# Kernel optimization log

Measured on AMD Instinct MI355X. Metric: run time of the kernel, lower is better.

The kernel has to match this reference:

```python
import jax, jax.numpy as jnp
import numpy as np


def setup_inputs() -> dict:
    key = jax.random.key(0)
    ks = jax.random.split(key, 7)
    B, D, d1, d2, d3 = 256, 256, 1024, 512, 256
    s = lambda f: 1.0 / np.sqrt(f)  # torch nn.Linear-style init scale
    return {
        "x": jax.random.normal(ks[0], (B, D), jnp.float32),
        "W1": jax.random.normal(ks[1], (d1, D), jnp.float32) * s(D),
        "b1": jax.random.normal(ks[2], (d1,), jnp.float32) * s(D),
        "W2": jax.random.normal(ks[3], (d2, d1), jnp.float32) * s(d1),
        "b2": jax.random.normal(ks[4], (d2,), jnp.float32) * s(d1),
        "W3": jax.random.normal(ks[5], (d3, d2), jnp.float32) * s(d2),
        "b3": jax.random.normal(ks[6], (d3,), jnp.float32) * s(d2),
        "k": 10,
    }


def _border_dists(x, W1, b1, W2, b2, W3, b3):
    # Layer 1: pre-activations and boundary distances. For the first layer the
    # effective linear map is W1 itself (shared across the batch).
    z1 = x @ W1.T + b1                                   # [B, d1]
    dist1 = jnp.abs(z1) / jnp.linalg.norm(W1, axis=1)    # [B, d1]
    m1 = (z1 > 0).astype(x.dtype)
    V1 = m1[:, :, None] * W1[None]                       # [B, d1, D] per-instance map after ReLU
    h1 = m1 * z1

    # Layer 2
    z2 = h1 @ W2.T + b2                                  # [B, d2]
    V2 = jnp.einsum('oi,bid->bod', W2, V1)               # [B, d2, D]
    dist2 = jnp.abs(z2) / jnp.linalg.norm(V2, axis=2)
    m2 = (z2 > 0).astype(x.dtype)
    h2 = m2 * z2

    # Layer 3
    z3 = h2 @ W3.T + b3                                  # [B, d3]
    V3 = jnp.einsum('oi,bid->bod', W3, m2[:, :, None] * V2)  # [B, d3, D]
    dist3 = jnp.abs(z3) / jnp.linalg.norm(V3, axis=2)

    return jnp.concatenate([dist1, dist2, dist3], axis=1)  # [B, d1+d2+d3]


def reference(x, W1, b1, W2, b2, W3, b3, k):
    dists = _border_dists(x, W1, b1, W2, b2, W3, b3)
    # smallest-k distances per instance via top_k on negated distances
    neg_top, _ = jax.lax.top_k(-dists, k)                # [B, k]
    return jnp.sum(-neg_top)                             # border-distance loss (scalar)
```

## Files before the change

### kernel.cpp

```cpp
#include <hip/hip_runtime.h>
#include <math.h>
#include <float.h>

#define B   256
#define D   256
#define D1  1024
#define D2  512
#define D3  256
#define NDIST (D1 + D2 + D3)
#define CQ  2.0f

typedef __attribute__((ext_vector_type(8))) short short8;
typedef __attribute__((ext_vector_type(4))) float f32x4;
typedef __attribute__((ext_vector_type(4))) int   i32x4;

__device__ __forceinline__ float waveReduceSum(float v) {
    #pragma unroll
    for (int off = 32; off > 0; off >>= 1)
        v += __shfl_down(v, off, 64);
    return v;
}
__device__ __forceinline__ float waveReduceMax(float v) {
    #pragma unroll
    for (int off = 32; off > 0; off >>= 1)
        v = fmaxf(v, __shfl_down(v, off, 64));
    return v;
}

__device__ __forceinline__ unsigned short f2bf(float f) {
    unsigned int u = __float_as_uint(f);
    u = (u + 0x7FFFu + ((u >> 16) & 1u)) >> 16;
    return (unsigned short)u;
}
__device__ __forceinline__ float bf2f(unsigned short h) {
    return __uint_as_float(((unsigned int)h) << 16);
}
__device__ __forceinline__ void gld16(const void* g, void* l) {
    __builtin_amdgcn_global_load_lds(
        (const __attribute__((address_space(1))) unsigned int*)g,
        (__attribute__((address_space(3))) unsigned int*)l, 16, 0, 0);
}

__device__ __forceinline__ int swz_src(int row, int lane) {
    return ((lane & 3) + ((row >> 1) & 3)) & 3;
}
__device__ __forceinline__ int swz_frag(int row, int quad) {
    return row * 32 + (((quad - ((row >> 1) & 3)) & 3) * 8);
}

__global__ __launch_bounds__(256) void k_prep(
    const float* __restrict__ x,  const float* __restrict__ W1,
    const float* __restrict__ W2, const float* __restrict__ W3,
    float* __restrict__ zeros,
    float* __restrict__ outp,
    unsigned short* __restrict__ xhi,  unsigned short* __restrict__ xlo,
    unsigned short* __restrict__ W1hi, unsigned short* __restrict__ W1lo,
    unsigned short* __restrict__ W2hi, unsigned short* __restrict__ W2lo,
    unsigned short* __restrict__ W3hi, unsigned short* __restrict__ W3lo,
    signed char* __restrict__ W1Ti8, float* __restrict__ saq,
    signed char* __restrict__ W2i8,  float* __restrict__ sbq,
    signed char* __restrict__ W3i8,  float* __restrict__ s3q,
    float* __restrict__ rn1) {
    int blk = blockIdx.x;
    int t = threadIdx.x;
    if (blk < 1536) {
        if (blk == 0 && t == 0) outp[0] = 0.f;
        zeros[blk * 256 + t] = 0.f;
        return;
    }
    if (blk < 2496) {
        int i4 = ((blk - 1536) * 256 + t) * 4;
        const float* src; unsigned short *hi, *lo; int off;
        if (i4 < 65536)       { src = x;  hi = xhi;  lo = xlo;  off = i4; }
        else if (i4 < 327680) { src = W1; hi = W1hi; lo = W1lo; off = i4 - 65536; }
        else if (i4 < 851968) { src = W2; hi = W2hi; lo = W2lo; off = i4 - 327680; }
        else                  { src = W3; hi = W3hi; lo = W3lo; off = i4 - 851968; }
        float4 v = *(const float4*)(src + off);
        ushort4 h, l;
        h.x = f2bf(v.x); l.x = f2bf(v.x - bf2f(h.x));
        h.y = f2bf(v.y); l.y = f2bf(v.y - bf2f(h.y));
        h.z = f2bf(v.z); l.z = f2bf(v.z - bf2f(h.z));
        h.w = f2bf(v.w); l.w = f2bf(v.w - bf2f(h.w));
        *(ushort4*)(hi + off) = h;
        *(ushort4*)(lo + off) = l;
        return;
    }
    if (blk < 2528) {
        int ty = t >> 5, tx = t & 31;
        int d = (blk - 2496) * 8 + ty;
        float m = 0.f;
        for (int i = tx; i < D1; i += 32) m = fmaxf(m, fabsf(W1[(size_t)i * D + d]));
        #pragma unroll
        for (int off = 16; off > 0; off >>= 1) m = fmaxf(m, __shfl_down(m, off, 32));
        m = __shfl(m, 0, 32);
        m = fmaxf(m, 1e-20f);
        if (tx == 0) saq[d] = m / 127.f;
        float inv = 127.f / m;
        for (int i = tx; i < D1; i += 32) {
            int q = __float2int_rn(W1[(size_t)i * D + d] * inv);
            W1Ti8[(size_t)d * D1 + i] = (signed char)q;
        }
        return;
    }
    if (blk < 2656) {
        int o = (blk - 2528) * 4 + (t >> 6);
        int l = t & 63;
        const float* row = W2 + (size_t)o * D1;
        float m = 0.f;
        for (int tt = l; tt < D1; tt += 64) m = fmaxf(m, fabsf(row[tt]));
        m = waveReduceMax(m);
        m = __shfl(m, 0, 64);
        m = fmaxf(m, 1e-20f);
        if (l == 0) sbq[o] = m / 127.f;
        float inv = 127.f / m;
        for (int tt = l; tt < D1; tt += 64)
            W2i8[(size_t)o * D1 + tt] = (signed char)__float2int_rn(row[tt] * inv);
        return;
    }
    if (blk < 2720) {
        int p = (blk - 2656) * 4 + (t >> 6);
        int l = t & 63;
        const float* row = W3 + (size_t)p * D2;
        float m = 0.f;
        for (int tt = l; tt < D2; tt += 64) m = fmaxf(m, fabsf(row[tt]));
        m = waveReduceMax(m);
        m = __shfl(m, 0, 64);
        m = fmaxf(m, 1e-20f);
        if (l == 0) s3q[p] = m / 127.f;
        float inv = 127.f / m;
        for (int tt = l; tt < D2; tt += 64)
            W3i8[(size_t)p * D2 + tt] = (signed char)__float2int_rn(row[tt] * inv);
        return;
    }
    {
        int gw = (blk - 2720) * 4 + (t >> 6);
        int lane = t & 63;
        const float* row = W1 + (size_t)gw * D;
        float s = 0.f;
        for (int tt = lane; tt < D; tt += 64) { float v = row[tt]; s += v * v; }
        s = waveReduceSum(s);
        if (lane == 0) rn1[gw] = sqrtf(s);
    }
}

template <int KD, int KL>
__device__ __forceinline__ void mfma3_64(
    const unsigned short* __restrict__ Ahi, const unsigned short* __restrict__ Alo,
    const unsigned short* __restrict__ Bhi, const unsigned short* __restrict__ Blo,
    int m0, int n0, int k0, unsigned short* sm, f32x4 acc[2][2]) {
    int tid = threadIdx.x;
    int l = tid & 63, w = tid >> 6;
    int rsub = l >> 2;
    int quad = l >> 4, l16 = l & 15;
    int wm = (w >> 1) * 32, wn = (w & 1) * 32;
    unsigned short* sAh = sm;
    unsigned short* sAl = sm + 2048;
    unsigned short* sBh = sm + 4096;
    unsigned short* sBl = sm + 6144;
    ptrdiff_t dA = Alo - Ahi, dB = Blo - Bhi;
    int rloc = w * 16 + rsub;
    int c = swz_src(rloc, l);
    const unsigned short* pa = Ahi + (size_t)(m0 + rloc) * KD + k0 + c * 8;
    const unsigned short* pb = Bhi + (size_t)(n0 + rloc) * KD + k0 + c * 8;
    int aoff[2], boff[2];
    #pragma unroll
    for (int mt = 0; mt < 2; mt++) aoff[mt] = swz_frag(wm + mt * 16 + l16, quad);
    #pragma unroll
    for (int nt = 0; nt < 2; nt++) boff[nt] = swz_frag(wn + nt * 16 + l16, quad);
    for (int kk = 0; kk < KL; kk += 32) {
        gld16(pa + kk,      sAh + w * 512);
        gld16(pa + dA + kk, sAl + w * 512);
        gld16(pb + kk,      sBh + w * 512);
        gld16(pb + dB + kk, sBl + w * 512);
        __syncthreads();
        short8 ah[2], al[2], bh[2], bl[2];
        #pragma unroll
        for (int mt = 0; mt < 2; mt++) {
            ah[mt] = *(const short8*)(sAh + aoff[mt]);
            al[mt] = *(const short8*)(sAl + aoff[mt]);
        }
        #pragma unroll
        for (int nt = 0; nt < 2; nt++) {
            bh[nt] = *(const short8*)(sBh + boff[nt]);
            bl[nt] = *(const short8*)(sBl + boff[nt]);
        }
        #pragma unroll
        for (int mt = 0; mt < 2; mt++)
            #pragma unroll
            for (int nt = 0; nt < 2; nt++) {
                acc[mt][nt] = __builtin_amdgcn_mfma_f32_16x16x32_bf16(ah[mt], bh[nt], acc[mt][nt], 0, 0, 0);
                acc[mt][nt] = __builtin_amdgcn_mfma_f32_16x16x32_bf16(ah[mt], bl[nt], acc[mt][nt], 0, 0, 0);
                acc[mt][nt] = __builtin_amdgcn_mfma_f32_16x16x32_bf16(al[mt], bh[nt], acc[mt][nt], 0, 0, 0);
            }
        __syncthreads();
    }
}

__global__ __launch_bounds__(256) void k_l1(
    const unsigned short* __restrict__ xhi,  const unsigned short* __restrict__ xlo,
    const unsigned short* __restrict__ W1hi, const unsigned short* __restrict__ W1lo,
    const float* __restrict__ b1, const float* __restrict__ rn1,
    float* __restrict__ dists, unsigned char* __restrict__ m1q,
    unsigned short* __restrict__ h1hi, unsigned short* __restrict__ h1lo) {
    __shared__ __align__(16) unsigned short sm[8192];
    int m0 = blockIdx.x * 64, n0 = blockIdx.y * 64;
    f32x4 acc[2][2] = {};
    mfma3_64<D, D>(xhi, xlo, W1hi, W1lo, m0, n0, 0, sm, acc);
    int l = threadIdx.x & 63, w = threadIdx.x >> 6;
    int quad = l >> 4, l16 = l & 15;
    int wm = (w >> 1) * 32, wn = (w & 1) * 32;
    #pragma unroll
    for (int mt = 0; mt < 2; mt++)
        #pragma unroll
        for (int nt = 0; nt < 2; nt++) {
            int n = n0 + wn + nt * 16 + l16;
            float bv = b1[n], rv = rn1[n];
            #pragma unroll
            for (int r = 0; r < 4; r++) {
                int m = m0 + wm + mt * 16 + quad * 4 + r;
                float z = acc[mt][nt][r] + bv;
                size_t idx = (size_t)m * D1 + n;
                dists[idx] = fabsf(z) / rv;
                m1q[idx] = (z > 0.f) ? 0xFFu : 0u;
                float h = z > 0.f ? z : 0.f;
                unsigned short hh = f2bf(h);
                h1hi[idx] = hh;
                h1lo[idx] = f2bf(h - bf2f(hh));
            }
        }
}

__global__ __launch_bounds__(256) void k_l2a(
    const unsigned short* __restrict__ h1hi, const unsigned short* __restrict__ h1lo,
    const unsigned short* __restrict__ W2hi, const unsigned short* __restrict__ W2lo,
    float* __restrict__ z2) {
    __shared__ __align__(16) unsigned short sm[8192];
    int m0 = blockIdx.x * 64, n0 = blockIdx.y * 64, k0 = blockIdx.z * 256;
    f32x4 acc[2][2] = {};
    mfma3_64<D1, 256>(h1hi, h1lo, W2hi, W2lo, m0, n0, k0, sm, acc);
    int l = threadIdx.x & 63, w = threadIdx.x >> 6;
    int quad = l >> 4, l16 = l & 15;
    int wm = (w >> 1) * 32, wn = (w & 1) * 32;
    #pragma unroll
    for (int mt = 0; mt < 2; mt++)
        #pragma unroll
        for (int nt = 0; nt < 2; nt++) {
            int n = n0 + wn + nt * 16 + l16;
            #pragma unroll
            for (int r = 0; r < 4; r++) {
                int m = m0 + wm + mt * 16 + quad * 4 + r;
                atomicAdd(&z2[(size_t)m * D2 + n], acc[mt][nt][r]);
            }
        }
}

__global__ __launch_bounds__(256) void k_l2b(
    const float* __restrict__ b2, float* __restrict__ z2,
    unsigned char* __restrict__ m2q,
    unsigned short* __restrict__ h2hi, unsigned short* __restrict__ h2lo) {
    int idx = blockIdx.x * 256 + threadIdx.x;
    int n = idx & (D2 - 1);
    float z = z2[idx] + b2[n];
    z2[idx] = z;
    m2q[idx] = (z > 0.f) ? 0xFFu : 0u;
    float h = z > 0.f ? z : 0.f;
    unsigned short hh = f2bf(h);
    h2hi[idx] = hh;
    h2lo[idx] = f2bf(h - bf2f(hh));
}

__global__ __launch_bounds__(256) void k_l3a(
    const unsigned short* __restrict__ h2hi, const unsigned short* __restrict__ h2lo,
    const unsigned short* __restrict__ W3hi, const unsigned short* __restrict__ W3lo,
    float* __restrict__ z3) {
    __shared__ __align__(16) unsigned short sm[8192];
    int m0 = blockIdx.x * 64, n0 = blockIdx.y * 64, k0 = blockIdx.z * 256;
    f32x4 acc[2][2] = {};
    mfma3_64<D2, 256>(h2hi, h2lo, W3hi, W3lo, m0, n0, k0, sm, acc);
    int l = threadIdx.x & 63, w = threadIdx.x >> 6;
    int quad = l >> 4, l16 = l & 15;
    int wm = (w >> 1) * 32, wn = (w & 1) * 32;
    #pragma unroll
    for (int mt = 0; mt < 2; mt++)
        #pragma unroll
        for (int nt = 0; nt < 2; nt++) {
            int n = n0 + wn + nt * 16 + l16;
            #pragma unroll
            for (int r = 0; r < 4; r++) {
                int m = m0 + wm + mt * 16 + quad * 4 + r;
                atomicAdd(&z3[(size_t)m * D3 + n], acc[mt][nt][r]);
            }
        }
}

__global__ __launch_bounds__(256) void k_l3b(
    const float* __restrict__ b3, float* __restrict__ z3) {
    int idx = blockIdx.x * 256 + threadIdx.x;
    z3[idx] = z3[idx] + b3[idx & (D3 - 1)];
}

__global__ __launch_bounds__(256) void k_gemm1(
    const signed char* __restrict__ W1Ti8,
    const signed char* __restrict__ W2i8,
    const unsigned char* __restrict__ m1q,
    const float* __restrict__ saq,
    const float* __restrict__ sbq,
    signed char* __restrict__ qV2,
    float* __restrict__ norm2,
    int b0) {
    __shared__ __align__(16) signed char As[16384];
    __shared__ __align__(16) signed char Bs[16384];
    int m0 = blockIdx.x * 128;
    int o0 = blockIdx.y * 128;
    int bc = blockIdx.z;
    int b = b0 + bc;
    int tid = threadIdx.x;
    int l = tid & 63, w = tid >> 6;
    int quad = l >> 4, l16 = l & 15;
    int wm = (w >> 1) * 64, wn = (w & 1) * 64;
    const unsigned char* mrow = m1q + (size_t)b * D1;

    const signed char* pa[4];
    const signed char* pb[4];
    int lrow = l >> 3, ls = l & 7;
    #pragma unroll
    for (int r = 0; r < 4; r++) {
        int row = r * 32 + w * 8 + lrow;
        int c = (ls + (row & 7)) & 7;
        pa[r] = W1Ti8 + (size_t)(m0 + row) * D1 + c * 16;
        pb[r] = W2i8 + (size_t)(o0 + row) * D1 + c * 16;
    }
    int aoff[4][2], boff[4][2];
    #pragma unroll
    for (int mt = 0; mt < 4; mt++) {
        int tr = wm + mt * 16 + l16;
        #pragma unroll
        for (int ks = 0; ks < 2; ks++)
            aoff[mt][ks] = tr * 128 + (((ks * 4 + quad) - (tr & 7)) & 7) * 16;
    }
    #pragma unroll
    for (int nt = 0; nt < 4; nt++) {
        int tr = wn + nt * 16 + l16;
        #pragma unroll
        for (int ks = 0; ks < 2; ks++)
            boff[nt][ks] = tr * 128 + (((ks * 4 + quad) - (tr & 7)) & 7) * 16;
    }

    i32x4 acc[4][4];
    #pragma unroll
    for (int i = 0; i < 4; i++)
        #pragma unroll
        for (int j = 0; j < 4; j++) acc[i][j] = (i32x4)0;

    for (int kk = 0; kk < D1; kk += 128) {
        #pragma unroll
        for (int r = 0; r < 4; r++) {
            gld16(pa[r] + kk, As + r * 4096 + w * 1024);
            gld16(pb[r] + kk, Bs + r * 4096 + w * 1024);
        }
        i32x4 mv0 = *(const i32x4*)(mrow + kk + quad * 16);
        i32x4 mv1 = *(const i32x4*)(mrow + kk + 64 + quad * 16);
        __syncthreads();
        #pragma unroll
        for (int ks = 0; ks < 2; ks++) {
            i32x4 mv = ks ? mv1 : mv0;
            i32x4 a[4], bq[4];
            #pragma unroll
            for (int mt = 0; mt < 4; mt++)
                a[mt] = (*(const i32x4*)(As + aoff[mt][ks])) & mv;
            #pragma unroll
            for (int nt = 0; nt < 4; nt++)
                bq[nt] = *(const i32x4*)(Bs + boff[nt][ks]);
            #pragma unroll
            for (int mt = 0; mt < 4; mt++)
                #pragma unroll
                for (int nt = 0; nt < 4; nt++)
                    acc[mt][nt] = __builtin_amdgcn_mfma_i32_16x16x64_i8(
                        a[mt], bq[nt], acc[mt][nt], 0, 0, 0);
        }
        __syncthreads();
    }

    float sad[4][4];
    #pragma unroll
    for (int mt = 0; mt < 4; mt++)
        #pragma unroll
        for (int r = 0; r < 4; r++)
            sad[mt][r] = saq[m0 + wm + mt * 16 + quad * 4 + r];
    float sbv[4], sbdq[4];
    #pragma unroll
    for (int nt = 0; nt < 4; nt++) {
        sbv[nt] = sbq[o0 + wn + nt * 16 + l16];
        sbdq[nt] = sbv[nt] * (1.0f / CQ);
    }

    #pragma unroll
    for (int nt = 0; nt < 4; nt++) {
        float s = 0.f;
        #pragma unroll
        for (int mt = 0; mt < 4; mt++)
            #pragma unroll
            for (int r = 0; r < 4; r++) {
                float v = (float)acc[mt][nt][r] * sad[mt][r] * sbv[nt];
                s += v * v;
            }
        s += __shfl_down(s, 32, 64);
        s += __shfl_down(s, 16, 64);
        if (l < 16)
            atomicAdd(&norm2[(size_t)b * D2 + o0 + wn + nt * 16 + l], s);
    }

    signed char* qb = qV2 + (size_t)bc * (D * D2);
    #pragma unroll
    for (int mt = 0; mt < 4; mt++) {
        int dbase = m0 + wm + mt * 16 + quad * 4;
        #pragma unroll
        for (int r = 0; r < 4; r++)
            #pragma unroll
            for (int nt = 0; nt < 4; nt++) {
                int o = o0 + wn + nt * 16 + l16;
                int qi = __float2int_rn((float)acc[mt][nt][r] * sbdq[nt]);
                qi = max(-127, min(127, qi));
                qb[(size_t)(dbase + r) * D2 + o] = (signed char)qi;
            }
    }
}

__global__ __launch_bounds__(256) void k_gemm2(
    const signed char* __restrict__ W3i8,
    const signed char* __restrict__ qV2,
    const unsigned char* __restrict__ m2q,
    const float* __restrict__ saq,
    const float* __restrict__ s3q,
    float* __restrict__ norm3,
    int b0) {
    __shared__ __align__(16) signed char As[16384];
    __shared__ __align__(16) signed char Bs[16384];
    int m0 = blockIdx.x * 128;
    int n0 = blockIdx.y * 128;
    int bc = blockIdx.z;
    int b = b0 + bc;
    int tid = threadIdx.x;
    int l = tid & 63, w = tid >> 6;
    int quad = l >> 4, l16 = l & 15;
    int wm = (w >> 1) * 64, wn = (w & 1) * 64;
    const unsigned char* mrow = m2q + (size_t)b * D2;
    const signed char* Bsrc = qV2 + (size_t)bc * (D * D2);

    const signed char* pa[4];
    const signed char* pb[4];
    int lrow = l >> 3, ls = l & 7;
    #pragma unroll
    for (int r = 0; r < 4; r++) {
        int row = r * 32 + w * 8 + lrow;
        int c = (ls + (row & 7)) & 7;
        pa[r] = W3i8 + (size_t)(m0 + row) * D2 + c * 16;
        pb[r] = Bsrc + (size_t)(n0 + row) * D2 + c * 16;
    }
    int aoff[4][2], boff[4][2];
    #pragma unroll
    for (int mt = 0; mt < 4; mt++) {
        int tr = wm + mt * 16 + l16;
        #pragma unroll
        for (int ks = 0; ks < 2; ks++)
            aoff[mt][ks] = tr * 128 + (((ks * 4 + quad) - (tr & 7)) & 7) * 16;
    }
    #pragma unroll
    for (int nt = 0; nt < 4; nt++) {
        int tr = wn + nt * 16 + l16;
        #pragma unroll
        for (int ks = 0; ks < 2; ks++)
            boff[nt][ks] = tr * 128 + (((ks * 4 + quad) - (tr & 7)) & 7) * 16;
    }

    i32x4 acc[4][4];
    #pragma unroll
    for (int i = 0; i < 4; i++)
        #pragma unroll
        for (int j = 0; j < 4; j++) acc[i][j] = (i32x4)0;

    for (int kk = 0; kk < D2; kk += 128) {
        #pragma unroll
        for (int r = 0; r < 4; r++) {
            gld16(pa[r] + kk, As + r * 4096 + w * 1024);
            gld16(pb[r] + kk, Bs + r * 4096 + w * 1024);
        }
        i32x4 mv0 = *(const i32x4*)(mrow + kk + quad * 16);
        i32x4 mv1 = *(const i32x4*)(mrow + kk + 64 + quad * 16);
        __syncthreads();
        #pragma unroll
        for (int ks = 0; ks < 2; ks++) {
            i32x4 mv = ks ? mv1 : mv0;
            i32x4 a[4], bq[4];
            #pragma unroll
            for (int mt = 0; mt < 4; mt++)
                a[mt] = *(const i32x4*)(As + aoff[mt][ks]);
            #pragma unroll
            for (int nt = 0; nt < 4; nt++)
                bq[nt] = (*(const i32x4*)(Bs + boff[nt][ks])) & mv;
            #pragma unroll
            for (int mt = 0; mt < 4; mt++)
                #pragma unroll
                for (int nt = 0; nt < 4; nt++)
                    acc[mt][nt] = __builtin_amdgcn_mfma_i32_16x16x64_i8(
                        a[mt], bq[nt], acc[mt][nt], 0, 0, 0);
        }
        __syncthreads();
    }

    float saCQ[4];
    #pragma unroll
    for (int nt = 0; nt < 4; nt++)
        saCQ[nt] = saq[n0 + wn + nt * 16 + l16] * CQ;

    #pragma unroll
    for (int mt = 0; mt < 4; mt++)
        #pragma unroll
        for (int r = 0; r < 4; r++) {
            float s = 0.f;
            #pragma unroll
            for (int nt = 0; nt < 4; nt++) {
                float v = (float)acc[mt][nt][r] * saCQ[nt];
                s += v * v;
            }
            s += __shfl_down(s, 8, 64);
            s += __shfl_down(s, 4, 64);
            s += __shfl_down(s, 2, 64);
            s += __shfl_down(s, 1, 64);
            if (l16 == 0) {
                int p = m0 + wm + mt * 16 + quad * 4 + r;
                float s3 = s3q[p];
                atomicAdd(&norm3[(size_t)b * D3 + p], s * s3 * s3);
            }
        }
}

__global__ __launch_bounds__(256) void k_topk(
    const float* __restrict__ dists,
    const float* __restrict__ z2, const float* __restrict__ norm2,
    const float* __restrict__ z3, const float* __restrict__ norm3,
    const int* __restrict__ kp, float* __restrict__ outp) {
    __shared__ unsigned long long wmin[4];
    int b = blockIdx.x, t = threadIdx.x;
    float lv[7];
    #pragma unroll
    for (int j = 0; j < 4; j++) lv[j] = dists[(size_t)b * D1 + t + 256 * j];
    #pragma unroll
    for (int j = 4; j < 6; j++) {
        int o = t + 256 * j - 1024;
        lv[j] = fabsf(z2[(size_t)b * D2 + o]) / sqrtf(norm2[(size_t)b * D2 + o]);
    }
    lv[6] = fabsf(z3[(size_t)b * D3 + t]) / sqrtf(norm3[(size_t)b * D3 + t]);
    int k = *kp;
    if (k > NDIST) k = NDIST;
    float sum = 0.f;
    for (int it = 0; it < k; it++) {
        float mv = lv[0]; int mj = 0;
        #pragma unroll
        for (int j = 1; j < 7; j++)
            if (lv[j] < mv) { mv = lv[j]; mj = j; }
        unsigned long long key =
            ((unsigned long long)__float_as_uint(mv) << 32) | (unsigned)(t * 8 + mj);
        #pragma unroll
        for (int off = 32; off > 0; off >>= 1) {
            unsigned long long o = __shfl_down(key, off, 64);
            if (o < key) key = o;
        }
        if ((t & 63) == 0) wmin[t >> 6] = key;
        __syncthreads();
        unsigned long long k0 = wmin[0];
        #pragma unroll
        for (int ww = 1; ww < 4; ww++) if (wmin[ww] < k0) k0 = wmin[ww];
        sum += __uint_as_float((unsigned)(k0 >> 32));
        int wt = (int)((k0 & 0xFFFu) >> 3), wj = (int)(k0 & 7u);
        if (t == wt) lv[wj] = FLT_MAX;
        __syncthreads();
    }
    if (t == 0) atomicAdd(outp, sum);
}

extern "C" void kernel_launch(void* const* d_in, const int* in_sizes, int n_in,
                              void* d_out, int out_size, void* d_ws, size_t ws_size,
                              hipStream_t stream) {
    const float* x  = (const float*)d_in[0];
    const float* W1 = (const float*)d_in[1];
    const float* b1 = (const float*)d_in[2];
    const float* W2 = (const float*)d_in[3];
    const float* b2 = (const float*)d_in[4];
    const float* W3 = (const float*)d_in[5];
    const float* b3 = (const float*)d_in[6];
    const int*   kp = (const int*)d_in[7];
    float* outp = (float*)d_out;

    float* fp = (float*)d_ws;
    float* rn1     = fp;                          fp += D1;
    float* dists   = fp;                          fp += (size_t)B * D1;
    float* saq     = fp;                          fp += D;
    float* sbq     = fp;                          fp += D2;
    float* s3q     = fp;                          fp += D3;
    float* z2      = fp;                          fp += (size_t)B * D2;
    float* z3      = fp;                          fp += (size_t)B * D3;
    float* norm2   = fp;                          fp += (size_t)B * D2;
    float* norm3   = fp;                          fp += (size_t)B * D3;
    unsigned short* up = (unsigned short*)fp;
    unsigned short* W2hi  = up;  up += (size_t)D2 * D1;
    unsigned short* W2lo  = up;  up += (size_t)D2 * D1;
    unsigned short* W3hi  = up;  up += (size_t)D3 * D2;
    unsigned short* W3lo  = up;  up += (size_t)D3 * D2;
    unsigned short* xhi   = up;  up += (size_t)B * D;
    unsigned short* xlo   = up;  up += (size_t)B * D;
    unsigned short* W1hi  = up;  up += (size_t)D1 * D;
    unsigned short* W1lo  = up;  up += (size_t)D1 * D;
    unsigned short* h1hi  = up;  up += (size_t)B * D1;
    unsigned short* h1lo  = up;  up += (size_t)B * D1;
    unsigned short* h2hi  = up;  up += (size_t)B * D2;
    unsigned short* h2lo  = up;  up += (size_t)B * D2;
    signed char*    cp = (signed char*)up;
    signed char*    W1Ti8 = cp;  cp += (size_t)D * D1;
    signed char*    W2i8  = cp;  cp += (size_t)D2 * D1;
    signed char*    W3i8  = cp;  cp += (size_t)D3 * D2;
    unsigned char*  m1q   = (unsigned char*)cp;  cp += (size_t)B * D1;
    unsigned char*  m2q   = (unsigned char*)cp;  cp += (size_t)B * D2;
    signed char*    qV2   = cp;

    size_t base_bytes = (size_t)((char*)qV2 - (char*)d_ws);
    int CH = 8;
    const int cands[6] = {256, 128, 64, 32, 16, 8};
    for (int c = 0; c < 6; c++) {
        size_t need = base_bytes + (size_t)cands[c] * D * D2;
        if (need <= ws_size) { CH = cands[c]; break; }
    }

    k_prep<<<2976, 256, 0, stream>>>(x, W1, W2, W3, z2, outp,
                                     xhi, xlo, W1hi, W1lo, W2hi, W2lo, W3hi, W3lo,
                                     W1Ti8, saq, W2i8, sbq, W3i8, s3q, rn1);

    k_l1<<<dim3(B / 64, D1 / 64), 256, 0, stream>>>(xhi, xlo, W1hi, W1lo, b1, rn1,
                                                    dists, m1q, h1hi, h1lo);
    k_l2a<<<dim3(B / 64, D2 / 64, 4), 256, 0, stream>>>(h1hi, h1lo, W2hi, W2lo, z2);
    k_l2b<<<(B * D2) / 256, 256, 0, stream>>>(b2, z2, m2q, h2hi, h2lo);
    k_l3a<<<dim3(B / 64, D3 / 64, 2), 256, 0, stream>>>(h2hi, h2lo, W3hi, W3lo, z3);
    k_l3b<<<(B * D3) / 256, 256, 0, stream>>>(b3, z3);

    for (int b0 = 0; b0 < B; b0 += CH) {
        k_gemm1<<<dim3(D / 128, D2 / 128, CH), 256, 0, stream>>>(
            W1Ti8, W2i8, m1q, saq, sbq, qV2, norm2, b0);
        k_gemm2<<<dim3(D3 / 128, D / 128, CH), 256, 0, stream>>>(
            W3i8, qV2, m2q, saq, s3q, norm3, b0);
    }

    k_topk<<<B, 256, 0, stream>>>(dists, z2, norm2, z3, norm3, kp, outp);
}
```

Before: 192.4 us.

## Merge layer GEMMs with per-instance Jacobian GEMMs into combined launches

Folds the split-K layer-2 forward GEMM into the same launch as the batched int8 Jacobian GEMM1, and the layer-3 forward GEMM into the launch with GEMM2. Block index ranges select which role a block plays. The bias add for z3 moves into the top-k kernel, which removes k_l3b. The batch-chunk loop is dropped and all 256 instances go in one launch, so fewer kernels are launched and the small forward GEMMs overlap with the large ones. The cost is that the workspace must now hold the full qV2 for all instances, with no size check.

New measurement: 180.7 us. 6.1% less time.

```diff
diff --git a/kernel.cpp b/kernel.cpp
--- a/kernel.cpp
+++ b/kernel.cpp
@@ -26,7 +26,6 @@
         v = fmaxf(v, __shfl_down(v, off, 64));
     return v;
 }
-
 __device__ __forceinline__ unsigned short f2bf(float f) {
     unsigned int u = __float_as_uint(f);
     u = (u + 0x7FFFu + ((u >> 16) & 1u)) >> 16;
@@ -40,7 +39,6 @@
         (const __attribute__((address_space(1))) unsigned int*)g,
         (__attribute__((address_space(3))) unsigned int*)l, 16, 0, 0);
 }
-
 __device__ __forceinline__ int swz_src(int row, int lane) {
     return ((lane & 3) + ((row >> 1) & 3)) & 3;
 }
@@ -230,28 +228,159 @@
         }
 }
 
-__global__ __launch_bounds__(256) void k_l2a(
+__global__ __launch_bounds__(256) void k_big1(
     const unsigned short* __restrict__ h1hi, const unsigned short* __restrict__ h1lo,
     const unsigned short* __restrict__ W2hi, const unsigned short* __restrict__ W2lo,
-    float* __restrict__ z2) {
-    __shared__ __align__(16) unsigned short sm[8192];
-    int m0 = blockIdx.x * 64, n0 = blockIdx.y * 64, k0 = blockIdx.z * 256;
-    f32x4 acc[2][2] = {};
-    mfma3_64<D1, 256>(h1hi, h1lo, W2hi, W2lo, m0, n0, k0, sm, acc);
-    int l = threadIdx.x & 63, w = threadIdx.x >> 6;
+    float* __restrict__ z2,
+    const signed char* __restrict__ W1Ti8,
+    const signed char* __restrict__ W2i8,
+    const unsigned char* __restrict__ m1q,
+    const float* __restrict__ saq,
+    const float* __restrict__ sbq,
+    signed char* __restrict__ qV2,
+    float* __restrict__ norm2) {
+    __shared__ __align__(16) unsigned char smem[32768];
+    int bid = blockIdx.x;
+
+    if (bid < 128) {
+        unsigned short* sm = (unsigned short*)smem;
+        int m0 = (bid & 3) * 64, n0 = ((bid >> 2) & 7) * 64, k0 = (bid >> 5) * 256;
+        f32x4 acc[2][2] = {};
+        mfma3_64<D1, 256>(h1hi, h1lo, W2hi, W2lo, m0, n0, k0, sm, acc);
+        int l = threadIdx.x & 63, w = threadIdx.x >> 6;
+        int quad = l >> 4, l16 = l & 15;
+        int wm = (w >> 1) * 32, wn = (w & 1) * 32;
+        #pragma unroll
+        for (int mt = 0; mt < 2; mt++)
+            #pragma unroll
+            for (int nt = 0; nt < 2; nt++) {
+                int n = n0 + wn + nt * 16 + l16;
+                #pragma unroll
+                for (int r = 0; r < 4; r++) {
+                    int m = m0 + wm + mt * 16 + quad * 4 + r;
+                    atomicAdd(&z2[(size_t)m * D2 + n], acc[mt][nt][r]);
+                }
+            }
+        return;
+    }
+
+    int j = bid - 128;
+    signed char* As = (signed char*)smem;
+    signed char* Bs = (signed char*)smem + 16384;
+    int m0 = (j & 1) * 128;
+    int o0 = ((j >> 1) & 3) * 128;
+    int bc = j >> 3;
+    int b = bc;
+    int tid = threadIdx.x;
+    int l = tid & 63, w = tid >> 6;
     int quad = l >> 4, l16 = l & 15;
-    int wm = (w >> 1) * 32, wn = (w & 1) * 32;
-    #pragma unroll
-    for (int mt = 0; mt < 2; mt++)
-        #pragma unroll
-        for (int nt = 0; nt < 2; nt++) {
-            int n = n0 + wn + nt * 16 + l16;
+    int wm = (w >> 1) * 64, wn = (w & 1) * 64;
+    const unsigned char* mrow = m1q + (size_t)b * D1;
+
+    const signed char* pa[4];
+    const signed char* pb[4];
+    int lrow = l >> 3, ls = l & 7;
+    #pragma unroll
+    for (int r = 0; r < 4; r++) {
+        int row = r * 32 + w * 8 + lrow;
+        int c = (ls + (row & 7)) & 7;
+        pa[r] = W1Ti8 + (size_t)(m0 + row) * D1 + c * 16;
+        pb[r] = W2i8 + (size_t)(o0 + row) * D1 + c * 16;
+    }
+    int aoff[4][2], boff[4][2];
+    #pragma unroll
+    for (int mt = 0; mt < 4; mt++) {
+        int tr = wm + mt * 16 + l16;
+        #pragma unroll
+        for (int ks = 0; ks < 2; ks++)
+            aoff[mt][ks] = tr * 128 + (((ks * 4 + quad) - (tr & 7)) & 7) * 16;
+    }
+    #pragma unroll
+    for (int nt = 0; nt < 4; nt++) {
+        int tr = wn + nt * 16 + l16;
+        #pragma unroll
+        for (int ks = 0; ks < 2; ks++)
+            boff[nt][ks] = tr * 128 + (((ks * 4 + quad) - (tr & 7)) & 7) * 16;
+    }
+
+    i32x4 acc[4][4];
+    #pragma unroll
+    for (int i = 0; i < 4; i++)
+        #pragma unroll
+        for (int jj = 0; jj < 4; jj++) acc[i][jj] = (i32x4)0;
+
+    for (int kk = 0; kk < D1; kk += 128) {
+        #pragma unroll
+        for (int r = 0; r < 4; r++) {
+            gld16(pa[r] + kk, As + r * 4096 + w * 1024);
+            gld16(pb[r] + kk, Bs + r * 4096 + w * 1024);
+        }
+        i32x4 mv0 = *(const i32x4*)(mrow + kk + quad * 16);
+        i32x4 mv1 = *(const i32x4*)(mrow + kk + 64 + quad * 16);
+        __syncthreads();
+        #pragma unroll
+        for (int ks = 0; ks < 2; ks++) {
+            i32x4 mv = ks ? mv1 : mv0;
+            i32x4 a[4], bq[4];
+            #pragma unroll
+            for (int mt = 0; mt < 4; mt++)
+                a[mt] = (*(const i32x4*)(As + aoff[mt][ks])) & mv;
+            #pragma unroll
+            for (int nt = 0; nt < 4; nt++)
+                bq[nt] = *(const i32x4*)(Bs + boff[nt][ks]);
+            #pragma unroll
+            for (int mt = 0; mt < 4; mt++)
+                #pragma unroll
+                for (int nt = 0; nt < 4; nt++)
+                    acc[mt][nt] = __builtin_amdgcn_mfma_i32_16x16x64_i8(
+                        a[mt], bq[nt], acc[mt][nt], 0, 0, 0);
+        }
+        __syncthreads();
+    }
+
+    float sad[4][4];
+    #pragma unroll
+    for (int mt = 0; mt < 4; mt++)
+        #pragma unroll
+        for (int r = 0; r < 4; r++)
+            sad[mt][r] = saq[m0 + wm + mt * 16 + quad * 4 + r];
+    float sbv[4], sbdq[4];
+    #pragma unroll
+    for (int nt = 0; nt < 4; nt++) {
+        sbv[nt] = sbq[o0 + wn + nt * 16 + l16];
+        sbdq[nt] = sbv[nt] * (1.0f / CQ);
+    }
+
+    #pragma unroll
+    for (int nt = 0; nt < 4; nt++) {
+        float s = 0.f;
+        #pragma unroll
+        for (int mt = 0; mt < 4; mt++)
             #pragma unroll
             for (int r = 0; r < 4; r++) {
-                int m = m0 + wm + mt * 16 + quad * 4 + r;
-                atomicAdd(&z2[(size_t)m * D2 + n], acc[mt][nt][r]);
-            }
-        }
+                float v = (float)acc[mt][nt][r] * sad[mt][r] * sbv[nt];
+                s += v * v;
+            }
+        s += __shfl_down(s, 32, 64);
+        s += __shfl_down(s, 16, 64);
+        if (l < 16)
+            atomicAdd(&norm2[(size_t)b * D2 + o0 + wn + nt * 16 + l], s);
+    }
+
+    signed char* qb = qV2 + (size_t)bc * (D * D2);
+    #pragma unroll
+    for (int mt = 0; mt < 4; mt++) {
+        int dbase = m0 + wm + mt * 16 + quad * 4;
+        #pragma unroll
+        for (int r = 0; r < 4; r++)
+            #pragma unroll
+            for (int nt = 0; nt < 4; nt++) {
+                int o = o0 + wn + nt * 16 + l16;
+                int qi = __float2int_rn((float)acc[mt][nt][r] * sbdq[nt]);
+                qi = max(-127, min(127, qi));
+                qb[(size_t)(dbase + r) * D2 + o] = (signed char)qi;
+            }
+    }
 }
 
 __global__ __launch_bounds__(256) void k_l2b(
@@ -269,177 +398,48 @@
     h2lo[idx] = f2bf(h - bf2f(hh));
 }
 
-__global__ __launch_bounds__(256) void k_l3a(
+__global__ __launch_bounds__(256) void k_big2(
     const unsigned short* __restrict__ h2hi, const unsigned short* __restrict__ h2lo,
     const unsigned short* __restrict__ W3hi, const unsigned short* __restrict__ W3lo,
-    float* __restrict__ z3) {
-    __shared__ __align__(16) unsigned short sm[8192];
-    int m0 = blockIdx.x * 64, n0 = blockIdx.y * 64, k0 = blockIdx.z * 256;
-    f32x4 acc[2][2] = {};
-    mfma3_64<D2, 256>(h2hi, h2lo, W3hi, W3lo, m0, n0, k0, sm, acc);
-    int l = threadIdx.x & 63, w = threadIdx.x >> 6;
-    int quad = l >> 4, l16 = l & 15;
-    int wm = (w >> 1) * 32, wn = (w & 1) * 32;
-    #pragma unroll
-    for (int mt = 0; mt < 2; mt++)
-        #pragma unroll
-        for (int nt = 0; nt < 2; nt++) {
-            int n = n0 + wn + nt * 16 + l16;
-            #pragma unroll
-            for (int r = 0; r < 4; r++) {
-                int m = m0 + wm + mt * 16 + quad * 4 + r;
-                atomicAdd(&z3[(size_t)m * D3 + n], acc[mt][nt][r]);
-            }
-        }
-}
-
-__global__ __launch_bounds__(256) void k_l3b(
-    const float* __restrict__ b3, float* __restrict__ z3) {
-    int idx = blockIdx.x * 256 + threadIdx.x;
-    z3[idx] = z3[idx] + b3[idx & (D3 - 1)];
-}
-
-__global__ __launch_bounds__(256) void k_gemm1(
-    const signed char* __restrict__ W1Ti8,
-    const signed char* __restrict__ W2i8,
-    const unsigned char* __restrict__ m1q,
-    const float* __restrict__ saq,
-    const float* __restrict__ sbq,
-    signed char* __restrict__ qV2,
-    float* __restrict__ norm2,
-    int b0) {
-    __shared__ __align__(16) signed char As[16384];
-    __shared__ __align__(16) signed char Bs[16384];
-    int m0 = blockIdx.x * 128;
-    int o0 = blockIdx.y * 128;
-    int bc = blockIdx.z;
-    int b = b0 + bc;
-    int tid = threadIdx.x;
-    int l = tid & 63, w = tid >> 6;
-    int quad = l >> 4, l16 = l & 15;
-    int wm = (w >> 1) * 64, wn = (w & 1) * 64;
-    const unsigned char* mrow = m1q + (size_t)b * D1;
-
-    const signed char* pa[4];
-    const signed char* pb[4];
-    int lrow = l >> 3, ls = l & 7;
-    #pragma unroll
-    for (int r = 0; r < 4; r++) {
-        int row = r * 32 + w * 8 + lrow;
-        int c = (ls + (row & 7)) & 7;
-        pa[r] = W1Ti8 + (size_t)(m0 + row) * D1 + c * 16;
-        pb[r] = W2i8 + (size_t)(o0 + row) * D1 + c * 16;
-    }
-    int aoff[4][2], boff[4][2];
-    #pragma unroll
-    for (int mt = 0; mt < 4; mt++) {
-        int tr = wm + mt * 16 + l16;
-        #pragma unroll
-        for (int ks = 0; ks < 2; ks++)
-            aoff[mt][ks] = tr * 128 + (((ks * 4 + quad) - (tr & 7)) & 7) * 16;
-    }
-    #pragma unroll
-    for (int nt = 0; nt < 4; nt++) {
-        int tr = wn + nt * 16 + l16;
-        #pragma unroll
-        for (int ks = 0; ks < 2; ks++)
-            boff[nt][ks] = tr * 128 + (((ks * 4 + quad) - (tr & 7)) & 7) * 16;
-    }
-
-    i32x4 acc[4][4];
-    #pragma unroll
-    for (int i = 0; i < 4; i++)
-        #pragma unroll
-        for (int j = 0; j < 4; j++) acc[i][j] = (i32x4)0;
-
-    for (int kk = 0; kk < D1; kk += 128) {
-        #pragma unroll
-        for (int r = 0; r < 4; r++) {
-            gld16(pa[r] + kk, As + r * 4096 + w * 1024);
-            gld16(pb[r] + kk, Bs + r * 4096 + w * 1024);
-        }
-        i32x4 mv0 = *(const i32x4*)(mrow + kk + quad * 16);
-        i32x4 mv1 = *(const i32x4*)(mrow + kk + 64 + quad * 16);
-        __syncthreads();
-        #pragma unroll
-        for (int ks = 0; ks < 2; ks++) {
-            i32x4 mv = ks ? mv1 : mv0;
-            i32x4 a[4], bq[4];
-            #pragma unroll
-            for (int mt = 0; mt < 4; mt++)
-                a[mt] = (*(const i32x4*)(As + aoff[mt][ks])) & mv;
-            #pragma unroll
-            for (int nt = 0; nt < 4; nt++)
-                bq[nt] = *(const i32x4*)(Bs + boff[nt][ks]);
-            #pragma unroll
-            for (int mt = 0; mt < 4; mt++)
-                #pragma unroll
-                for (int nt = 0; nt < 4; nt++)
-                    acc[mt][nt] = __builtin_amdgcn_mfma_i32_16x16x64_i8(
-                        a[mt], bq[nt], acc[mt][nt], 0, 0, 0);
-        }
-        __syncthreads();
-    }
-
-    float sad[4][4];
-    #pragma unroll
-    for (int mt = 0; mt < 4; mt++)
-        #pragma unroll
-        for (int r = 0; r < 4; r++)
-            sad[mt][r] = saq[m0 + wm + mt * 16 + quad * 4 + r];
-    float sbv[4], sbdq[4];
-    #pragma unroll
-    for (int nt = 0; nt < 4; nt++) {
-        sbv[nt] = sbq[o0 + wn + nt * 16 + l16];
-        sbdq[nt] = sbv[nt] * (1.0f / CQ);
-    }
-
-    #pragma unroll
-    for (int nt = 0; nt < 4; nt++) {
-        float s = 0.f;
-        #pragma unroll
-        for (int mt = 0; mt < 4; mt++)
-            #pragma unroll
-            for (int r = 0; r < 4; r++) {
-                float v = (float)acc[mt][nt][r] * sad[mt][r] * sbv[nt];
-                s += v * v;
-            }
-        s += __shfl_down(s, 32, 64);
-        s += __shfl_down(s, 16, 64);
-        if (l < 16)
-            atomicAdd(&norm2[(size_t)b * D2 + o0 + wn + nt * 16 + l], s);
-    }
-
-    signed char* qb = qV2 + (size_t)bc * (D * D2);
-    #pragma unroll
-    for (int mt = 0; mt < 4; mt++) {
-        int dbase = m0 + wm + mt * 16 + quad * 4;
-        #pragma unroll
-        for (int r = 0; r < 4; r++)
-            #pragma unroll
-            for (int nt = 0; nt < 4; nt++) {
-                int o = o0 + wn + nt * 16 + l16;
-                int qi = __float2int_rn((float)acc[mt][nt][r] * sbdq[nt]);
-                qi = max(-127, min(127, qi));
-                qb[(size_t)(dbase + r) * D2 + o] = (signed char)qi;
-            }
-    }
-}
-
-__global__ __launch_bounds__(256) void k_gemm2(
+    float* __restrict__ z3,
     const signed char* __restrict__ W3i8,
     const signed char* __restrict__ qV2,
     const unsigned char* __restrict__ m2q,
     const float* __restrict__ saq,
     const float* __restrict__ s3q,
-    float* __restrict__ norm3,
-    int b0) {
-    __shared__ __align__(16) signed char As[16384];
-    __shared__ __align__(16) signed char Bs[16384];
-    int m0 = blockIdx.x * 128;
-    int n0 = blockIdx.y * 128;
-    int bc = blockIdx.z;
-    int b = b0 + bc;
+    float* __restrict__ norm3) {
+    __shared__ __align__(16) unsigned char smem[32768];
+    int bid = blockIdx.x;
+
+    if (bid < 32) {
+        unsigned short* sm = (unsigned short*)smem;
+        int m0 = (bid & 3) * 64, n0 = ((bid >> 2) & 3) * 64, k0 = (bid >> 4) * 256;
+        f32x4 acc[2][2] = {};
+        mfma3_64<D2, 256>(h2hi, h2lo, W3hi, W3lo, m0, n0, k0, sm, acc);
+        int l = threadIdx.x & 63, w = threadIdx.x >> 6;
+        int quad = l >> 4, l16 = l & 15;
+        int wm = (w >> 1) * 32, wn = (w & 1) * 32;
+        #pragma unroll
+        for (int mt = 0; mt < 2; mt++)
+            #pragma unroll
+            for (int nt = 0; nt < 2; nt++) {
+                int n = n0 + wn + nt * 16 + l16;
+                #pragma unroll
+                for (int r = 0; r < 4; r++) {
+                    int m = m0 + wm + mt * 16 + quad * 4 + r;
+                    atomicAdd(&z3[(size_t)m * D3 + n], acc[mt][nt][r]);
+                }
+            }
+        return;
+    }
+
+    int j = bid - 32;
+    signed char* As = (signed char*)smem;
+    signed char* Bs = (signed char*)smem + 16384;
+    int m0 = (j & 1) * 128;
+    int n0 = ((j >> 1) & 1) * 128;
+    int bc = j >> 2;
+    int b = bc;
     int tid = threadIdx.x;
     int l = tid & 63, w = tid >> 6;
     int quad = l >> 4, l16 = l & 15;
@@ -477,7 +477,7 @@
     #pragma unroll
     for (int i = 0; i < 4; i++)
         #pragma unroll
-        for (int j = 0; j < 4; j++) acc[i][j] = (i32x4)0;
+        for (int jj = 0; jj < 4; jj++) acc[i][jj] = (i32x4)0;
 
     for (int kk = 0; kk < D2; kk += 128) {
         #pragma unroll
@@ -538,7 +538,8 @@
 __global__ __launch_bounds__(256) void k_topk(
     const float* __restrict__ dists,
     const float* __restrict__ z2, const float* __restrict__ norm2,
-    const float* __restrict__ z3, const float* __restrict__ norm3,
+    const float* __restrict__ z3, const float* __restrict__ b3,
+    const float* __restrict__ norm3,
     const int* __restrict__ kp, float* __restrict__ outp) {
     __shared__ unsigned long long wmin[4];
     int b = blockIdx.x, t = threadIdx.x;
@@ -550,7 +551,10 @@
         int o = t + 256 * j - 1024;
         lv[j] = fabsf(z2[(size_t)b * D2 + o]) / sqrtf(norm2[(size_t)b * D2 + o]);
     }
-    lv[6] = fabsf(z3[(size_t)b * D3 + t]) / sqrtf(norm3[(size_t)b * D3 + t]);
+    {
+        float zz = z3[(size_t)b * D3 + t] + b3[t];
+        lv[6] = fabsf(zz) / sqrtf(norm3[(size_t)b * D3 + t]);
+    }
     int k = *kp;
     if (k > NDIST) k = NDIST;
     float sum = 0.f;
@@ -623,31 +627,20 @@
     unsigned char*  m2q   = (unsigned char*)cp;  cp += (size_t)B * D2;
     signed char*    qV2   = cp;
 
-    size_t base_bytes = (size_t)((char*)qV2 - (char*)d_ws);
-    int CH = 8;
-    const int cands[6] = {256, 128, 64, 32, 16, 8};
-    for (int c = 0; c < 6; c++) {
-        size_t need = base_bytes + (size_t)cands[c] * D * D2;
-        if (need <= ws_size) { CH = cands[c]; break; }
-    }
-
     k_prep<<<2976, 256, 0, stream>>>(x, W1, W2, W3, z2, outp,
                                      xhi, xlo, W1hi, W1lo, W2hi, W2lo, W3hi, W3lo,
                                      W1Ti8, saq, W2i8, sbq, W3i8, s3q, rn1);
 
     k_l1<<<dim3(B / 64, D1 / 64), 256, 0, stream>>>(xhi, xlo, W1hi, W1lo, b1, rn1,
                                                     dists, m1q, h1hi, h1lo);
-    k_l2a<<<dim3(B / 64, D2 / 64, 4), 256, 0, stream>>>(h1hi, h1lo, W2hi, W2lo, z2);
+
+    k_big1<<<2176, 256, 0, stream>>>(h1hi, h1lo, W2hi, W2lo, z2,
+                                     W1Ti8, W2i8, m1q, saq, sbq, qV2, norm2);
+
     k_l2b<<<(B * D2) / 256, 256, 0, stream>>>(b2, z2, m2q, h2hi, h2lo);
-    k_l3a<<<dim3(B / 64, D3 / 64, 2), 256, 0, stream>>>(h2hi, h2lo, W3hi, W3lo, z3);
-    k_l3b<<<(B * D3) / 256, 256, 0, stream>>>(b3, z3);
-
-    for (int b0 = 0; b0 < B; b0 += CH) {
-        k_gemm1<<<dim3(D / 128, D2 / 128, CH), 256, 0, stream>>>(
-            W1Ti8, W2i8, m1q, saq, sbq, qV2, norm2, b0);
-        k_gemm2<<<dim3(D3 / 128, D / 128, CH), 256, 0, stream>>>(
-            W3i8, qV2, m2q, saq, s3q, norm3, b0);
-    }
-
-    k_topk<<<B, 256, 0, stream>>>(dists, z2, norm2, z3, norm3, kp, outp);
-}
+
+    k_big2<<<1056, 256, 0, stream>>>(h2hi, h2lo, W3hi, W3lo, z3,
+                                     W3i8, qV2, m2q, saq, s3q, norm3);
+
+    k_topk<<<B, 256, 0, stream>>>(dists, z2, norm2, z3, b3, norm3, kp, outp);
+}
```
